# Optimization experiments

Hardware: AMD Instinct MI355X
Metric: run time of the kernel (lower is better)

Reference implementation:

```python
import jax, jax.numpy as jnp
import numpy as np

HEAD_SIZE = 64  # n_embds // n_heads = 1024 // 16

def setup_inputs() -> dict:
    key = jax.random.key(0)
    k0, k1, k2, k3 = jax.random.split(key, 4)
    B, S, D, H = 4, 4096, 1024, HEAD_SIZE
    scale = 1.0 / np.sqrt(D)
    return {
        "decoder_input": jax.random.normal(k0, (B, S, D), dtype=jnp.float32),
        "Wq": jax.random.normal(k1, (D, H), dtype=jnp.float32) * scale,
        "Wk": jax.random.normal(k2, (D, H), dtype=jnp.float32) * scale,
        "Wv": jax.random.normal(k3, (D, H), dtype=jnp.float32) * scale,
    }

def reference(decoder_input, Wq, Wk, Wv):
    # q,k,v: [B,S,H]; Linear(bias=False) == x @ W
    q = decoder_input @ Wq
    k = decoder_input @ Wk
    v = decoder_input @ Wv
    head_size = k.shape[2]
    # scores: [B,S,S] -- full materialization, as in the original
    scores = jnp.einsum('bqh,bkh->bqk', q, k) / jnp.sqrt(jnp.float32(head_size))
    S = scores.shape[1]
    causal = jnp.tril(jnp.ones((S, S), dtype=bool))  # lower-triangular mask
    masked = jnp.where(causal, scores, -jnp.inf)
    attn = jax.nn.softmax(masked, axis=2)
    # dropout_rate = 0.0 -> identity
    return jnp.einsum('bqk,bkh->bqh', attn, v)
```

## Files before the change

kernel.cpp:

```cpp
#include <hip/hip_runtime.h>
#include <hip/hip_bf16.h>
#include <math.h>

typedef __bf16 bf16_t;
typedef __bf16 bf16x8 __attribute__((ext_vector_type(8)));
typedef float f32x4 __attribute__((ext_vector_type(4)));

constexpr int SS = 4096;
constexpr int DD = 1024;
constexpr int HH = 64;

#if __has_builtin(__builtin_amdgcn_exp2f)
#define EXP2F __builtin_amdgcn_exp2f
#else
#define EXP2F exp2f
#endif

static __device__ __forceinline__ f32x4 mfma16(bf16x8 a, bf16x8 b, f32x4 c) {
  return __builtin_amdgcn_mfma_f32_16x16x32_bf16(a, b, c, 0, 0, 0);
}

__global__ __launch_bounds__(256) void prep_w(const float* __restrict__ wq,
                                              const float* __restrict__ wk,
                                              const float* __restrict__ wv,
                                              bf16_t* __restrict__ wt) {
  __shared__ float ls[64 * 68];
  int tid = threadIdx.x;
  int sel = blockIdx.x >> 4, kb = blockIdx.x & 15, k0 = kb * 64;
  const float* src = (sel == 0) ? wq : ((sel == 1) ? wk : wv);
  int bn = sel * 64;
#pragma unroll
  for (int i = 0; i < 4; ++i) {
    int e = tid + i * 256;
    int r = e >> 4, c4 = (e & 15) * 4;
    *(float4*)&ls[r * 68 + c4] = *(const float4*)(src + (size_t)(k0 + r) * 64 + c4);
  }
  __syncthreads();
#pragma unroll
  for (int j = 0; j < 2; ++j) {
    int e = tid + j * 256;
    int n = e >> 3, kg = e & 7;
    bf16x8 v;
#pragma unroll
    for (int t = 0; t < 8; ++t) v[t] = (bf16_t)ls[(kg * 8 + t) * 68 + n];
    *(bf16x8*)(wt + (size_t)(bn + n) * 1024 + k0 + kg * 8) = v;
  }
}

__global__ __launch_bounds__(256) void gemm_qkv(const float* __restrict__ x,
                                                const bf16_t* __restrict__ wt,
                                                bf16_t* __restrict__ qo,
                                                bf16_t* __restrict__ ko,
                                                bf16_t* __restrict__ vto) {
  __shared__ bf16_t xs[2][64 * 64];
  __shared__ bf16_t wsh[2][96 * 64];
  int tid = threadIdx.x;
  int wave = tid >> 6, lane = tid & 63, quad = lane >> 4, ml = lane & 15;
  int mblk = blockIdx.x >> 1, nhalf = blockIdx.x & 1;
  int m0 = mblk * 64;
  int nbase = nhalf * 96;

  f32x4 acc[6];
#pragma unroll
  for (int i = 0; i < 6; ++i) acc[i] = (f32x4){0.f, 0.f, 0.f, 0.f};

  int xrow = tid >> 2, xseg = tid & 3;
  float4 xr[4];
  bf16x8 wr[3];

  auto load_g = [&](int k0) {
    const float* p = x + (size_t)(m0 + xrow) * DD + k0 + xseg * 16;
    xr[0] = *(const float4*)p;
    xr[1] = *(const float4*)(p + 4);
    xr[2] = *(const float4*)(p + 8);
    xr[3] = *(const float4*)(p + 12);
#pragma unroll
    for (int i = 0; i < 3; ++i) {
      int c = tid + i * 256;
      int r = c >> 3, cc = c & 7;
      wr[i] = *(const bf16x8*)(wt + (size_t)(nbase + r) * DD + k0 + cc * 8);
    }
  };
  auto store_lds = [&](int bf) {
    bf16x8 v0, v1;
    v0[0] = (bf16_t)xr[0].x; v0[1] = (bf16_t)xr[0].y;
    v0[2] = (bf16_t)xr[0].z; v0[3] = (bf16_t)xr[0].w;
    v0[4] = (bf16_t)xr[1].x; v0[5] = (bf16_t)xr[1].y;
    v0[6] = (bf16_t)xr[1].z; v0[7] = (bf16_t)xr[1].w;
    v1[0] = (bf16_t)xr[2].x; v1[1] = (bf16_t)xr[2].y;
    v1[2] = (bf16_t)xr[2].z; v1[3] = (bf16_t)xr[2].w;
    v1[4] = (bf16_t)xr[3].x; v1[5] = (bf16_t)xr[3].y;
    v1[6] = (bf16_t)xr[3].z; v1[7] = (bf16_t)xr[3].w;
    int cc0 = (2 * xseg) ^ (xrow & 7);
    int cc1 = (2 * xseg + 1) ^ (xrow & 7);
    *(bf16x8*)&xs[bf][xrow * 64 + cc0 * 8] = v0;
    *(bf16x8*)&xs[bf][xrow * 64 + cc1 * 8] = v1;
#pragma unroll
    for (int i = 0; i < 3; ++i) {
      int c = tid + i * 256;
      int r = c >> 3, cc = c & 7;
      *(bf16x8*)&wsh[bf][r * 64 + ((cc ^ (r & 7)) * 8)] = wr[i];
    }
  };

  load_g(0);
  store_lds(0);
  load_g(64);
  __syncthreads();
  for (int it = 0; it < 16; ++it) {
    int bf = it & 1;
#pragma unroll
    for (int s = 0; s < 2; ++s) {
      int rchunk = ((s * 4 + quad) ^ (ml & 7)) * 8;
      bf16x8 a = *(const bf16x8*)&xs[bf][(wave * 16 + ml) * 64 + rchunk];
#pragma unroll
      for (int i = 0; i < 6; ++i) {
        bf16x8 bfr = *(const bf16x8*)&wsh[bf][(i * 16 + ml) * 64 + rchunk];
        acc[i] = mfma16(a, bfr, acc[i]);
      }
    }
    if (it < 15) {
      store_lds(1 - bf);
      if (it < 14) load_g((it + 2) * 64);
      __syncthreads();
    }
  }

  int b = m0 >> 12;
  int sr = m0 & 4095;
  const float QSCALE = 0.18033688011112042f;
  bf16_t* vls = (bf16_t*)wsh;
#pragma unroll
  for (int i = 0; i < 6; ++i) {
    int col = nbase + i * 16 + ml;
#pragma unroll
    for (int r = 0; r < 4; ++r) {
      int lrow = wave * 16 + quad * 4 + r;
      size_t grow = (size_t)b * SS + sr + lrow;
      if (col < 64) qo[grow * HH + col] = (bf16_t)(acc[i][r] * QSCALE);
      else if (col < 128) ko[grow * HH + (col - 64)] = (bf16_t)(acc[i][r]);
      else vls[(col - 128) * 72 + lrow] = (bf16_t)(acc[i][r]);
    }
  }
  __syncthreads();
  if (nhalf == 1) {
    int h = tid >> 2, sg = tid & 3;
    *(bf16x8*)(vto + ((size_t)b * HH + h) * SS + sr + sg * 16) =
        *(const bf16x8*)&vls[h * 72 + sg * 16];
    *(bf16x8*)(vto + ((size_t)b * HH + h) * SS + sr + sg * 16 + 8) =
        *(const bf16x8*)&vls[h * 72 + sg * 16 + 8];
  }
}

__global__ __launch_bounds__(256) void attn_partial(const bf16_t* __restrict__ qg,
                                                    const bf16_t* __restrict__ kg,
                                                    const bf16_t* __restrict__ vg,
                                                    float* __restrict__ partO,
                                                    float* __restrict__ lb,
                                                    float* __restrict__ out) {
  __shared__ bf16_t Kl[64 * 64];
  __shared__ bf16_t Vl[64 * 64];
  __shared__ bf16_t Pl[4][16 * 64];
  int tid = threadIdx.x;
  int wave = tid >> 6, lane = tid & 63, quad = lane >> 4, ml = lane & 15;

  int bid = blockIdx.x;
  int b = bid & 3;
  int j = 343 - (bid >> 2);
  int jt, ch, nch;
  if (j < 8)        { jt = j;                   ch = 0;            nch = 1; }
  else if (j < 24)  { jt = 8  + ((j - 8) >> 1); ch = (j - 8) & 1;  nch = 2; }
  else if (j < 88)  { jt = 16 + ((j - 24) >> 2); ch = (j - 24) & 3; nch = 4; }
  else              { jt = 32 + ((j - 88) >> 3); ch = (j - 88) & 7; nch = 8; }
  int L = (jt + nch) / nch;
  int c0 = ch * L;
  int c1 = c0 + L; if (c1 > jt + 1) c1 = jt + 1;
  int len = c1 - c0;
  bool direct = (nch == 1);
  int slot = b * 336 + (j - 8);
  int q0 = jt * 64;

  const bf16_t* qb = qg + (size_t)b * SS * HH;
  const bf16_t* kb = kg + (size_t)b * SS * HH;
  const bf16_t* vb = vg + (size_t)b * HH * SS;

  int qrow = q0 + wave * 16 + ml;
  bf16x8 aq0 = *(const bf16x8*)(qb + (size_t)qrow * HH + quad * 8);
  bf16x8 aq1 = *(const bf16x8*)(qb + (size_t)qrow * HH + 32 + quad * 8);

  bf16x8 kreg[2], vreg[2];
  int srl = tid >> 3, scc = tid & 7;
  auto load_kv = [&](int kt) {
#pragma unroll
    for (int i = 0; i < 2; ++i) {
      int r = srl + i * 32;
      kreg[i] = *(const bf16x8*)(kb + (size_t)(kt * 64 + r) * HH + scc * 8);
      vreg[i] = *(const bf16x8*)(vb + (size_t)r * SS + kt * 64 + scc * 8);
    }
  };
  auto store_kv = [&]() {
#pragma unroll
    for (int i = 0; i < 2; ++i) {
      int r = srl + i * 32;
      int off = r * 64 + ((scc ^ (r & 7)) * 8);
      *(bf16x8*)&Kl[off] = kreg[i];
      *(bf16x8*)&Vl[off] = vreg[i];
    }
  };

  f32x4 oa[4];
#pragma unroll
  for (int i = 0; i < 4; ++i) oa[i] = (f32x4){0.f, 0.f, 0.f, 0.f};
  float lr[4] = {0.f, 0.f, 0.f, 0.f};

  load_kv(c0);

  for (int i = 0; i < len; ++i) {
    int kt = c0 + i;
    __syncthreads();
    store_kv();
    __syncthreads();
    if (i + 1 < len) load_kv(kt + 1);

    f32x4 sa[4];
#pragma unroll
    for (int nt = 0; nt < 4; ++nt) sa[nt] = (f32x4){0.f, 0.f, 0.f, 0.f};
#pragma unroll
    for (int s = 0; s < 2; ++s) {
      bf16x8 a = s ? aq1 : aq0;
      int rchunk = ((s * 4 + quad) ^ (ml & 7)) * 8;
#pragma unroll
      for (int nt = 0; nt < 4; ++nt) {
        bf16x8 bfr = *(const bf16x8*)&Kl[(nt * 16 + ml) * 64 + rchunk];
        sa[nt] = mfma16(a, bfr, sa[nt]);
      }
    }

    if (kt == jt) {
#pragma unroll
      for (int nt = 0; nt < 4; ++nt) {
        int key = kt * 64 + nt * 16 + ml;
#pragma unroll
        for (int r = 0; r < 4; ++r) {
          int qr = q0 + wave * 16 + quad * 4 + r;
          if (key > qr) sa[nt][r] = -3.38953139e38f;
        }
      }
    }

#pragma unroll
    for (int r = 0; r < 4; ++r) {
      float p0 = EXP2F(sa[0][r]);
      float p1 = EXP2F(sa[1][r]);
      float p2 = EXP2F(sa[2][r]);
      float p3 = EXP2F(sa[3][r]);
      sa[0][r] = p0; sa[1][r] = p1; sa[2][r] = p2; sa[3][r] = p3;
      lr[r] += (p0 + p1) + (p2 + p3);
    }

#pragma unroll
    for (int nt = 0; nt < 4; ++nt) {
#pragma unroll
      for (int r = 0; r < 4; ++r) {
        int row = quad * 4 + r;
        int cc = nt * 2 + (ml >> 3);
        Pl[wave][row * 64 + ((cc ^ (row & 7)) * 8) + (ml & 7)] = (bf16_t)sa[nt][r];
      }
    }
#pragma unroll
    for (int s = 0; s < 2; ++s) {
      int rchunk = ((s * 4 + quad) ^ (ml & 7)) * 8;
      bf16x8 pa = *(const bf16x8*)&Pl[wave][ml * 64 + rchunk];
#pragma unroll
      for (int ht = 0; ht < 4; ++ht) {
        bf16x8 bv = *(const bf16x8*)&Vl[(ht * 16 + ml) * 64 + rchunk];
        oa[ht] = mfma16(pa, bv, oa[ht]);
      }
    }
  }

#pragma unroll
  for (int r = 0; r < 4; ++r) {
    float t = lr[r];
    t += __shfl_xor(t, 1);
    t += __shfl_xor(t, 2);
    t += __shfl_xor(t, 4);
    t += __shfl_xor(t, 8);
    lr[r] = t;
  }

  if (direct) {
#pragma unroll
    for (int r = 0; r < 4; ++r) {
      float inv = 1.0f / lr[r];
      int row = q0 + wave * 16 + quad * 4 + r;
#pragma unroll
      for (int ht = 0; ht < 4; ++ht)
        out[((size_t)b * SS + row) * HH + ht * 16 + ml] = oa[ht][r] * inv;
    }
  } else {
    float* po = partO + (size_t)slot * 4096;
#pragma unroll
    for (int r = 0; r < 4; ++r) {
      int row = wave * 16 + quad * 4 + r;
#pragma unroll
      for (int ht = 0; ht < 4; ++ht)
        po[row * 64 + ht * 16 + ml] = oa[ht][r];
      if (ml == 0) lb[slot * 64 + row] = lr[r];
    }
  }
}

__global__ __launch_bounds__(256) void combine(const float* __restrict__ partO,
                                               const float* __restrict__ lb,
                                               float* __restrict__ out) {
  int bid = blockIdx.x;
  int b = bid / 56;
  int jt = 8 + (bid - b * 56);
  int nch, jbase;
  if (jt < 16)      { nch = 2; jbase = 8 + 2 * (jt - 8); }
  else if (jt < 32) { nch = 4; jbase = 24 + 4 * (jt - 16); }
  else              { nch = 8; jbase = 88 + 8 * (jt - 32); }
  int base = b * 336 + (jbase - 8);
  int tid = threadIdx.x;
  int row = tid >> 2, cb = tid & 3;

  float l = 0.f;
  f32x4 o[4];
#pragma unroll
  for (int jj = 0; jj < 4; ++jj) o[jj] = (f32x4){0.f, 0.f, 0.f, 0.f};
  for (int c = 0; c < nch; ++c) {
    l += lb[(base + c) * 64 + row];
    const f32x4* p = (const f32x4*)(partO + (size_t)(base + c) * 4096 + row * 64 + cb * 16);
#pragma unroll
    for (int jj = 0; jj < 4; ++jj) o[jj] += p[jj];
  }
  float inv = 1.0f / l;
  f32x4* op = (f32x4*)(out + (((size_t)b * SS) + jt * 64 + row) * HH + cb * 16);
#pragma unroll
  for (int jj = 0; jj < 4; ++jj) op[jj] = o[jj] * inv;
}

extern "C" void kernel_launch(void* const* d_in, const int* in_sizes, int n_in,
                              void* d_out, int out_size, void* d_ws, size_t ws_size,
                              hipStream_t stream) {
  const float* x  = (const float*)d_in[0];
  const float* wq = (const float*)d_in[1];
  const float* wk = (const float*)d_in[2];
  const float* wv = (const float*)d_in[3];
  float* out = (float*)d_out;

  char* wsb = (char*)d_ws;
  bf16_t* wt  = (bf16_t*)wsb;
  bf16_t* q   = (bf16_t*)(wsb + 524288);
  bf16_t* k   = (bf16_t*)(wsb + 2621440);
  bf16_t* vt  = (bf16_t*)(wsb + 4718592);
  float*  po  = (float*)(wsb + 6815744);
  float*  lb  = (float*)(wsb + 28835840);

  prep_w<<<48, 256, 0, stream>>>(wq, wk, wv, wt);
  gemm_qkv<<<512, 256, 0, stream>>>(x, wt, q, k, vt);
  attn_partial<<<1376, 256, 0, stream>>>(q, k, vt, po, lb, out);
  combine<<<224, 256, 0, stream>>>(po, lb, out);
}
```

Before: 147.8 us.

## Fuse split-KV combine into attention via atomic last-block reduction with bf16 partials

Removes the separate combine kernel. Each split-KV attention block now writes its partial output in bf16 and increments a per-tile atomic counter, and the last block to arrive reduces all partials and writes the normalized result. This cuts one kernel launch, the fp32 partial traffic, and the tail of the combine pass. In exchange it adds a memset, fences and an atomic, and it lowers the precision of the partial sums.

```diff
diff --git a/kernel.cpp b/kernel.cpp
--- a/kernel.cpp
+++ b/kernel.cpp
@@ -155,12 +155,14 @@
 __global__ __launch_bounds__(256) void attn_partial(const bf16_t* __restrict__ qg,
                                                     const bf16_t* __restrict__ kg,
                                                     const bf16_t* __restrict__ vg,
-                                                    float* __restrict__ partO,
+                                                    bf16_t* __restrict__ partO,
                                                     float* __restrict__ lb,
-                                                    float* __restrict__ out) {
+                                                    float* __restrict__ out,
+                                                    int* __restrict__ cnt) {
   __shared__ bf16_t Kl[64 * 64];
   __shared__ bf16_t Vl[64 * 64];
   __shared__ bf16_t Pl[4][16 * 64];
+  __shared__ int s_last;
   int tid = threadIdx.x;
   int wave = tid >> 6, lane = tid & 63, quad = lane >> 4, ml = lane & 15;
 
@@ -168,10 +170,10 @@
   int b = bid & 3;
   int j = 343 - (bid >> 2);
   int jt, ch, nch;
-  if (j < 8)        { jt = j;                   ch = 0;            nch = 1; }
-  else if (j < 24)  { jt = 8  + ((j - 8) >> 1); ch = (j - 8) & 1;  nch = 2; }
-  else if (j < 88)  { jt = 16 + ((j - 24) >> 2); ch = (j - 24) & 3; nch = 4; }
-  else              { jt = 32 + ((j - 88) >> 3); ch = (j - 88) & 7; nch = 8; }
+  if (j < 8)        { jt = j;                    ch = 0;             nch = 1; }
+  else if (j < 24)  { jt = 8  + ((j - 8) >> 1);  ch = (j - 8) & 1;   nch = 2; }
+  else if (j < 88)  { jt = 16 + ((j - 24) >> 2); ch = (j - 24) & 3;  nch = 4; }
+  else              { jt = 32 + ((j - 88) >> 3); ch = (j - 88) & 7;  nch = 8; }
   int L = (jt + nch) / nch;
   int c0 = ch * L;
   int c1 = c0 + L; if (c1 > jt + 1) c1 = jt + 1;
@@ -298,47 +300,64 @@
       for (int ht = 0; ht < 4; ++ht)
         out[((size_t)b * SS + row) * HH + ht * 16 + ml] = oa[ht][r] * inv;
     }
-  } else {
-    float* po = partO + (size_t)slot * 4096;
+    return;
+  }
+
+  {
+    bf16x8 w0, w1;
+#pragma unroll
+    for (int ht = 0; ht < 2; ++ht)
+#pragma unroll
+      for (int r = 0; r < 4; ++r) w0[ht * 4 + r] = (bf16_t)oa[ht][r];
+#pragma unroll
+    for (int ht = 2; ht < 4; ++ht)
+#pragma unroll
+      for (int r = 0; r < 4; ++r) w1[(ht - 2) * 4 + r] = (bf16_t)oa[ht][r];
+    bf16_t* po = partO + (size_t)slot * 4096 + tid * 16;
+    *(bf16x8*)po = w0;
+    *(bf16x8*)(po + 8) = w1;
+    if (ml == 0) {
+#pragma unroll
+      for (int r = 0; r < 4; ++r)
+        lb[slot * 64 + wave * 16 + quad * 4 + r] = lr[r];
+    }
+  }
+  __syncthreads();
+  if (tid == 0) {
+    __builtin_amdgcn_fence(__ATOMIC_RELEASE, "agent");
+    s_last = __hip_atomic_fetch_add(&cnt[b * 64 + jt], 1, __ATOMIC_RELAXED,
+                                    __HIP_MEMORY_SCOPE_AGENT);
+  }
+  __syncthreads();
+  if (s_last == nch - 1) {
+    __builtin_amdgcn_fence(__ATOMIC_ACQUIRE, "agent");
+    int slot0 = slot - ch;
+    float a16[16];
+#pragma unroll
+    for (int t = 0; t < 16; ++t) a16[t] = 0.f;
+    float ls[4] = {0.f, 0.f, 0.f, 0.f};
+    for (int c = 0; c < nch; ++c) {
+      const bf16_t* pp = partO + (size_t)(slot0 + c) * 4096 + tid * 16;
+      bf16x8 r0 = *(const bf16x8*)pp;
+      bf16x8 r1 = *(const bf16x8*)(pp + 8);
+#pragma unroll
+      for (int t = 0; t < 8; ++t) {
+        a16[t] += (float)r0[t];
+        a16[8 + t] += (float)r1[t];
+      }
+#pragma unroll
+      for (int r = 0; r < 4; ++r)
+        ls[r] += lb[(slot0 + c) * 64 + wave * 16 + quad * 4 + r];
+    }
 #pragma unroll
     for (int r = 0; r < 4; ++r) {
-      int row = wave * 16 + quad * 4 + r;
+      float inv = 1.0f / ls[r];
+      int row = q0 + wave * 16 + quad * 4 + r;
 #pragma unroll
       for (int ht = 0; ht < 4; ++ht)
-        po[row * 64 + ht * 16 + ml] = oa[ht][r];
-      if (ml == 0) lb[slot * 64 + row] = lr[r];
-    }
-  }
-}
-
-__global__ __launch_bounds__(256) void combine(const float* __restrict__ partO,
-                                               const float* __restrict__ lb,
-                                               float* __restrict__ out) {
-  int bid = blockIdx.x;
-  int b = bid / 56;
-  int jt = 8 + (bid - b * 56);
-  int nch, jbase;
-  if (jt < 16)      { nch = 2; jbase = 8 + 2 * (jt - 8); }
-  else if (jt < 32) { nch = 4; jbase = 24 + 4 * (jt - 16); }
-  else              { nch = 8; jbase = 88 + 8 * (jt - 32); }
-  int base = b * 336 + (jbase - 8);
-  int tid = threadIdx.x;
-  int row = tid >> 2, cb = tid & 3;
-
-  float l = 0.f;
-  f32x4 o[4];
-#pragma unroll
-  for (int jj = 0; jj < 4; ++jj) o[jj] = (f32x4){0.f, 0.f, 0.f, 0.f};
-  for (int c = 0; c < nch; ++c) {
-    l += lb[(base + c) * 64 + row];
-    const f32x4* p = (const f32x4*)(partO + (size_t)(base + c) * 4096 + row * 64 + cb * 16);
-#pragma unroll
-    for (int jj = 0; jj < 4; ++jj) o[jj] += p[jj];
-  }
-  float inv = 1.0f / l;
-  f32x4* op = (f32x4*)(out + (((size_t)b * SS) + jt * 64 + row) * HH + cb * 16);
-#pragma unroll
-  for (int jj = 0; jj < 4; ++jj) op[jj] = o[jj] * inv;
+        out[((size_t)b * SS + row) * HH + ht * 16 + ml] = a16[ht * 4 + r] * inv;
+    }
+  }
 }
 
 extern "C" void kernel_launch(void* const* d_in, const int* in_sizes, int n_in,
@@ -355,11 +374,12 @@
   bf16_t* q   = (bf16_t*)(wsb + 524288);
   bf16_t* k   = (bf16_t*)(wsb + 2621440);
   bf16_t* vt  = (bf16_t*)(wsb + 4718592);
-  float*  po  = (float*)(wsb + 6815744);
-  float*  lb  = (float*)(wsb + 28835840);
-
+  bf16_t* po  = (bf16_t*)(wsb + 6815744);
+  float*  lb  = (float*)(wsb + 17825792);
+  int*   cnt  = (int*)(wsb + 18350080);
+
+  hipMemsetAsync(cnt, 0, 1024, stream);
   prep_w<<<48, 256, 0, stream>>>(wq, wk, wv, wt);
   gemm_qkv<<<512, 256, 0, stream>>>(x, wt, q, k, vt);
-  attn_partial<<<1376, 256, 0, stream>>>(q, k, vt, po, lb, out);
-  combine<<<224, 256, 0, stream>>>(po, lb, out);
-}
+  attn_partial<<<1376, 256, 0, stream>>>(q, k, vt, po, lb, out, cnt);
+}
```

Measured after the change: 187.8 us. 1.27x slower.
